# Optimization experiments

Hardware: AMD Instinct MI355X
Metric: run time of the kernel (lower is better)

## Reference

```python
import jax, jax.numpy as jnp
import numpy as np

MARGIN = 0.5
POS_WEIGHT = 0.5
NEG_WEIGHT = 0.5
PUNISHMENT_SCALE = 2.0
POS_THRESHOLD = 0.6
NEG_THRESHOLD = 0.3
BIG = 1e9  # finite sentinel instead of inf (grad-safe under where)


def setup_inputs() -> dict:
    key = jax.random.key(0)
    k1, k2, k3 = jax.random.split(key, 3)
    N, D = 8192, 256
    embeddings = jax.random.normal(k1, (N, D), dtype=jnp.float32)
    labels = jax.random.randint(k2, (N,), 0, 2, dtype=jnp.int32)
    pids = jax.random.randint(k3, (N,), 0, 256, dtype=jnp.int32)
    return {"embeddings": embeddings, "labels": labels, "pids": pids}


def reference(embeddings, labels, pids):
    N = embeddings.shape[0]
    # F.normalize(p=2, dim=1): x / max(||x||, eps)
    norm = jnp.maximum(jnp.linalg.norm(embeddings, axis=1, keepdims=True), 1e-12)
    normed = embeddings / norm
    sim = normed @ normed.T  # (N, N) cosine similarity

    same_pid = pids[:, None] == pids[None, :]            # (N, N)
    genuine_j = (labels == 1)[None, :]                   # (1, N)
    not_self = ~jnp.eye(N, dtype=bool)
    pos_mask = same_pid & genuine_j & not_self           # same pid, genuine, not anchor
    neg_mask = (same_pid & ~genuine_j) | ~same_pid       # same-pid forgeries or cross-pid

    valid = (labels == 1) & pos_mask.any(axis=1) & neg_mask.any(axis=1)

    # hardest positive = min similarity among positives
    hp = jnp.min(jnp.where(pos_mask, sim, BIG), axis=1)  # (N,)

    # semi-hard negatives: hp - margin < sim < hp
    semi = neg_mask & (sim < hp[:, None]) & (sim > (hp - MARGIN)[:, None])
    cand = neg_mask & (sim > hp[:, None])                # harder-than-positive negatives
    hn_semi = jnp.max(jnp.where(semi, sim, -BIG), axis=1)
    hn_cand = jnp.max(jnp.where(cand, sim, -BIG), axis=1)
    hn_all = jnp.max(jnp.where(neg_mask, sim, -BIG), axis=1)
    hn = jnp.where(semi.any(axis=1), hn_semi,
                   jnp.where(cand.any(axis=1), hn_cand, hn_all))

    base = jax.nn.relu(hn - hp + MARGIN)
    weight = jnp.where((hp < POS_THRESHOLD) | (hn > NEG_THRESHOLD),
                       PUNISHMENT_SCALE, 1.0)
    loss = base * weight + POS_WEIGHT * (1.0 - hp) + NEG_WEIGHT * jax.nn.relu(hn + 0.2)

    cnt = jnp.sum(valid)
    total = jnp.sum(jnp.where(valid, loss, 0.0))
    return jnp.where(cnt > 0, total / jnp.maximum(cnt, 1), 0.0)
```

## Files before the change

### kernel.cpp

```cpp
#include <hip/hip_runtime.h>
#include <hip/hip_bf16.h>
#include <stdint.h>

typedef __attribute__((ext_vector_type(8))) short short8;
typedef __attribute__((ext_vector_type(4))) float f32x4;

#define BIGF 1e9f
#define NSLOT 64
#define MAXM 96

__device__ inline float blo(unsigned int u) {
    union { unsigned int i; float f; } v; v.i = u << 16; return v.f;
}
__device__ inline float bhi(unsigned int u) {
    union { unsigned int i; float f; } v; v.i = u & 0xffff0000u; return v.f;
}
__device__ inline unsigned int fkey(float s) {
    unsigned int b = __float_as_uint(s);
    return (b & 0x80000000u) ? ~b : (b | 0x80000000u);
}
__device__ inline float funkey(unsigned int k) {
    unsigned int b = (k & 0x80000000u) ? (k & 0x7fffffffu) : ~k;
    return __uint_as_float(b);
}
__device__ inline void async16(const unsigned short* g, unsigned short* l) {
    __builtin_amdgcn_global_load_lds(
        (const __attribute__((address_space(1))) void*)g,
        (__attribute__((address_space(3))) void*)l, 16, 0, 0);
}
__device__ inline unsigned short f2b(float x) {
    __hip_bfloat16 h = __float2bfloat16(x);
    return *reinterpret_cast<unsigned short*>(&h);
}

__global__ __launch_bounds__(256) void k_normalize(
    const float* __restrict__ emb, const int* __restrict__ labels,
    const int* __restrict__ pids, unsigned short* __restrict__ normed,
    int* __restrict__ gpid, float* __restrict__ hp_init,
    float* __restrict__ gred, int* __restrict__ done)
{
    if (blockIdx.x == 0 && threadIdx.x < 3) {
        if (threadIdx.x < 2) gred[threadIdx.x] = 0.f;
        else *done = 0;
    }
    int w = threadIdx.x >> 6, lane = threadIdx.x & 63;
    int row = blockIdx.x * 4 + w;
    const float4* src = (const float4*)(emb + ((size_t)row << 8));
    float4 x = src[lane];
    float ss = x.x * x.x + x.y * x.y + x.z * x.z + x.w * x.w;
    #pragma unroll
    for (int off = 32; off >= 1; off >>= 1) ss += __shfl_xor(ss, off, 64);
    float inv = 1.0f / fmaxf(sqrtf(ss), 1e-12f);
    ushort4 o;
    o.x = f2b(x.x * inv); o.y = f2b(x.y * inv);
    o.z = f2b(x.z * inv); o.w = f2b(x.w * inv);
    ((ushort4*)(normed + ((size_t)row << 8)))[lane] = o;
    if (lane == 0) {
        gpid[row] = (labels[row] == 1) ? pids[row] : -1;
        hp_init[row] = BIGF;
    }
}

__global__ __launch_bounds__(256) void k_hp_pid(
    const unsigned short* __restrict__ normed, const int* __restrict__ labels,
    const int* __restrict__ pids, float* __restrict__ hp_out, int N, int D)
{
    __shared__ int list[MAXM];
    __shared__ unsigned int hp_loc[MAXM];
    __shared__ unsigned short rows[MAXM * 256];
    __shared__ int cnt;
    int p = blockIdx.x;
    int t = threadIdx.x;
    if (t == 0) cnt = 0;
    __syncthreads();
    for (int j = t; j < N; j += 256)
        if (pids[j] == p && labels[j] == 1) {
            int idx = atomicAdd(&cnt, 1);
            if (idx < MAXM) list[idx] = j;
        }
    __syncthreads();
    int M = min(cnt, MAXM);
    for (int s = t; s < M; s += 256) hp_loc[s] = 0xFFFFFFFFu;
    for (int idx = t; idx < M * 32; idx += 256) {
        int mi = idx >> 5, ch = idx & 31;
        ((uint4*)&rows[mi * 256])[ch] =
            ((const uint4*)(normed + ((size_t)list[mi] << 8)))[ch];
    }
    __syncthreads();
    for (int pr = t; pr < M * M; pr += 256) {
        int i = pr / M, j = pr - i * M;
        if (i == j) continue;
        const uint4* ap = (const uint4*)&rows[i * 256];
        const uint4* bp = (const uint4*)&rows[j * 256];
        float s = 0.f;
        #pragma unroll 4
        for (int k = 0; k < 32; ++k) {
            uint4 a = ap[k], b = bp[k];
            s += blo(a.x) * blo(b.x) + bhi(a.x) * bhi(b.x);
            s += blo(a.y) * blo(b.y) + bhi(a.y) * bhi(b.y);
            s += blo(a.z) * blo(b.z) + bhi(a.z) * bhi(b.z);
            s += blo(a.w) * blo(b.w) + bhi(a.w) * bhi(b.w);
        }
        atomicMin(&hp_loc[i], fkey(s));
    }
    __syncthreads();
    for (int s = t; s < M; s += 256) {
        unsigned int key = hp_loc[s];
        hp_out[list[s]] = (key == 0xFFFFFFFFu) ? BIGF : funkey(key);
    }
}

__global__ __launch_bounds__(256) void k_pass2(
    const unsigned short* __restrict__ normed, const int* __restrict__ pids,
    const int* __restrict__ gpid, const float* __restrict__ hp,
    float* __restrict__ p_hnall, float* __restrict__ p_mbel, int N)
{
    const int b = blockIdx.x;
    int rt = (int)floorf((129.0f - sqrtf(16641.0f - 8.0f * (float)b)) * 0.5f);
    rt = min(rt, 63);
    while (64 * (rt + 1) - ((rt + 1) * rt) / 2 <= b) ++rt;
    while (64 * rt - (rt * (rt - 1)) / 2 > b) --rt;
    const int ct = rt + (b - (64 * rt - (rt * (rt - 1)) / 2));
    const bool diag = (ct == rt);

    __shared__ unsigned short As[2][128 * 32];
    __shared__ unsigned short Bs[2][128 * 32];
    __shared__ float hp_r[128], hp_c[128];
    __shared__ int pid_r[128], gpid_r[128], pid_c[128], gpid_c[128];
    __shared__ unsigned int red1[128], red2[128], red3[128], red4[128];

    const int t = threadIdx.x;
    const int lane = t & 63;
    const int w = t >> 6;
    const int wr = w & 1, wc = w >> 1;
    const int quad = lane >> 4, l16 = lane & 15;
    const int rbase = rt * 128, cbase = ct * 128;

    if (t < 128) {
        hp_r[t] = hp[rbase + t];
        pid_r[t] = pids[rbase + t];
        gpid_r[t] = gpid[rbase + t];
        hp_c[t] = hp[cbase + t];
        pid_c[t] = pids[cbase + t];
        gpid_c[t] = gpid[cbase + t];
        red1[t] = 0u; red2[t] = 0u; red3[t] = 0u; red4[t] = 0u;
    }

    const int r0 = t >> 2, p0 = t & 3;
    const int c0 = p0 ^ ((r0 >> 1) & 3);
    const unsigned short* gA0 = normed + ((size_t)(rbase + r0) << 8) + c0 * 8;
    const unsigned short* gA1 = normed + ((size_t)(rbase + r0 + 64) << 8) + c0 * 8;
    const unsigned short* gB0 = normed + ((size_t)(cbase + r0) << 8) + c0 * 8;
    const unsigned short* gB1 = normed + ((size_t)(cbase + r0 + 64) << 8) + c0 * 8;

    async16(gA0, &As[0][t * 8]);
    async16(gA1, &As[0][2048 + t * 8]);
    if (!diag) {
        async16(gB0, &Bs[0][t * 8]);
        async16(gB1, &Bs[0][2048 + t * 8]);
    }

    f32x4 acc[4][4];
    #pragma unroll
    for (int mt = 0; mt < 4; ++mt)
        #pragma unroll
        for (int nt = 0; nt < 4; ++nt)
            acc[mt][nt] = (f32x4){0.f, 0.f, 0.f, 0.f};

    const int sw = (l16 >> 1) & 3;
    const int aoff = (wr * 64 + l16) * 32 + (quad ^ sw) * 8;
    const int boff = (wc * 64 + l16) * 32 + (quad ^ sw) * 8;

    const unsigned short* Bbase[2] = { diag ? &As[0][0] : &Bs[0][0],
                                       diag ? &As[1][0] : &Bs[1][0] };

    for (int kb = 0; kb < 8; ++kb) {
        __syncthreads();
        int cur = kb & 1;
        if (kb < 7) {
            int nxt = cur ^ 1;
            int ko = (kb + 1) << 5;
            async16(gA0 + ko, &As[nxt][t * 8]);
            async16(gA1 + ko, &As[nxt][2048 + t * 8]);
            if (!diag) {
                async16(gB0 + ko, &Bs[nxt][t * 8]);
                async16(gB1 + ko, &Bs[nxt][2048 + t * 8]);
            }
        }
        short8 af[4], bf[4];
        #pragma unroll
        for (int mt = 0; mt < 4; ++mt)
            af[mt] = *reinterpret_cast<const short8*>(&As[cur][aoff + mt * 512]);
        #pragma unroll
        for (int nt = 0; nt < 4; ++nt)
            bf[nt] = *reinterpret_cast<const short8*>(&Bbase[cur][boff + nt * 512]);
        #pragma unroll
        for (int mt = 0; mt < 4; ++mt)
            #pragma unroll
            for (int nt = 0; nt < 4; ++nt)
                acc[mt][nt] = __builtin_amdgcn_mfma_f32_16x16x32_bf16(
                    af[mt], bf[nt], acc[mt][nt], 0, 0, 0);
    }

    int gp[4];
    #pragma unroll
    for (int nt = 0; nt < 4; ++nt) gp[nt] = gpid_c[wc * 64 + nt * 16 + l16];
    #pragma unroll
    for (int mt = 0; mt < 4; ++mt) {
        #pragma unroll
        for (int r = 0; r < 4; ++r) {
            int rl = wr * 64 + mt * 16 + quad * 4 + r;
            int prow = pid_r[rl];
            float hprow = hp_r[rl];
            float v1 = -BIGF, v2 = -BIGF;
            #pragma unroll
            for (int nt = 0; nt < 4; ++nt) {
                float s = acc[mt][nt][r];
                float tt = (prow != gp[nt]) ? s : -BIGF;
                v1 = fmaxf(v1, tt);
                float t2 = (tt < hprow) ? tt : -BIGF;
                v2 = fmaxf(v2, t2);
            }
            #pragma unroll
            for (int off = 8; off >= 1; off >>= 1) {
                v1 = fmaxf(v1, __shfl_xor(v1, off, 64));
                v2 = fmaxf(v2, __shfl_xor(v2, off, 64));
            }
            if (l16 == 0) {
                atomicMax(&red1[rl], fkey(v1));
                atomicMax(&red2[rl], fkey(v2));
            }
        }
    }

    if (!diag) {
        int4 gr[4];
        #pragma unroll
        for (int mt = 0; mt < 4; ++mt)
            gr[mt] = *(const int4*)&gpid_r[wr * 64 + mt * 16 + quad * 4];
        #pragma unroll
        for (int nt = 0; nt < 4; ++nt) {
            int c = wc * 64 + nt * 16 + l16;
            int pc = pid_c[c];
            float hpc = hp_c[c];
            float v1 = -BIGF, v2 = -BIGF;
            #pragma unroll
            for (int mt = 0; mt < 4; ++mt) {
                const int* g = (const int*)&gr[mt];
                #pragma unroll
                for (int r = 0; r < 4; ++r) {
                    float s = acc[mt][nt][r];
                    float tt = (pc != g[r]) ? s : -BIGF;
                    v1 = fmaxf(v1, tt);
                    float t2 = (tt < hpc) ? tt : -BIGF;
                    v2 = fmaxf(v2, t2);
                }
            }
            v1 = fmaxf(v1, __shfl_xor(v1, 16, 64));
            v1 = fmaxf(v1, __shfl_xor(v1, 32, 64));
            v2 = fmaxf(v2, __shfl_xor(v2, 16, 64));
            v2 = fmaxf(v2, __shfl_xor(v2, 32, 64));
            if (quad == 0) {
                atomicMax(&red3[c], fkey(v1));
                atomicMax(&red4[c], fkey(v2));
            }
        }
    }

    __syncthreads();
    if (t < 128) {
        p_hnall[(size_t)ct * N + rbase + t] = funkey(red1[t]);
        p_mbel[(size_t)ct * N + rbase + t] = funkey(red2[t]);
        if (!diag) {
            p_hnall[(size_t)rt * N + cbase + t] = funkey(red3[t]);
            p_mbel[(size_t)rt * N + cbase + t] = funkey(red4[t]);
        }
    }
}

__global__ __launch_bounds__(256) void k_rowloss(
    const float* __restrict__ hp, const float* __restrict__ p_hnall,
    const float* __restrict__ p_mbel, const int* __restrict__ labels,
    float* __restrict__ gred, int* __restrict__ done,
    float* __restrict__ out, int N)
{
    int i = blockIdx.x * 256 + threadIdx.x;
    float hn_all = -BIGF, mb = -BIGF;
    #pragma unroll 8
    for (int s = 0; s < NSLOT; ++s) {
        hn_all = fmaxf(hn_all, p_hnall[(size_t)s * N + i]);
        mb = fmaxf(mb, p_mbel[(size_t)s * N + i]);
    }
    float hpv = hp[i];
    bool valid = (labels[i] == 1) && (hpv < 1e8f) && (hn_all > -1e8f);
    float hn = (mb > hpv - 0.5f) ? mb : hn_all;
    float base = fmaxf(hn - hpv + 0.5f, 0.f);
    float wgt = (hpv < 0.6f || hn > 0.3f) ? 2.f : 1.f;
    float loss = base * wgt + 0.5f * (1.f - hpv) + 0.5f * fmaxf(hn + 0.2f, 0.f);
    float lsum = valid ? loss : 0.f;
    float lcnt = valid ? 1.f : 0.f;
    #pragma unroll
    for (int off = 32; off >= 1; off >>= 1) {
        lsum += __shfl_xor(lsum, off, 64);
        lcnt += __shfl_xor(lcnt, off, 64);
    }
    __shared__ float rs[4], rc[4];
    int wv = threadIdx.x >> 6, lane = threadIdx.x & 63;
    if (lane == 0) { rs[wv] = lsum; rc[wv] = lcnt; }
    __syncthreads();
    if (threadIdx.x == 0) {
        atomicAdd(&gred[0], rs[0] + rs[1] + rs[2] + rs[3]);
        atomicAdd(&gred[1], rc[0] + rc[1] + rc[2] + rc[3]);
        __threadfence();
        int old = atomicAdd(done, 1);
        if (old == (int)gridDim.x - 1) {
            float S = atomicAdd(&gred[0], 0.f);
            float C = atomicAdd(&gred[1], 0.f);
            out[0] = (C > 0.f) ? S / fmaxf(C, 1.f) : 0.f;
        }
    }
}

extern "C" void kernel_launch(void* const* d_in, const int* in_sizes, int n_in,
                              void* d_out, int out_size, void* d_ws, size_t ws_size,
                              hipStream_t stream)
{
    const float* emb = (const float*)d_in[0];
    const int* labels = (const int*)d_in[1];
    const int* pids = (const int*)d_in[2];
    float* out = (float*)d_out;
    int N = in_sizes[1];
    int D = in_sizes[0] / N;

    char* ws = (char*)d_ws;
    unsigned short* normed = (unsigned short*)ws;  ws += (size_t)N * D * 2;
    int* gpid = (int*)ws;                          ws += (size_t)N * 4;
    float* hp = (float*)ws;                        ws += (size_t)N * 4;
    float* p_hnall = (float*)ws;                   ws += (size_t)N * NSLOT * 4;
    float* p_mbel = (float*)ws;                    ws += (size_t)N * NSLOT * 4;
    float* gred = (float*)ws;                      ws += 2 * 4;
    int* done = (int*)ws;                          ws += 4;

    int M = N / 128;
    int tri = M * (M + 1) / 2;

    k_normalize<<<N / 4, 256, 0, stream>>>(emb, labels, pids, normed, gpid, hp,
                                           gred, done);
    k_hp_pid<<<256, 256, 0, stream>>>(normed, labels, pids, hp, N, D);
    k_pass2<<<tri, 256, 0, stream>>>(normed, pids, gpid, hp,
                                     p_hnall, p_mbel, N);
    k_rowloss<<<N / 256, 256, 0, stream>>>(hp, p_hnall, p_mbel, labels,
                                           gred, done, out, N);
}
```

Measured before the change: 150.0 us.

## Fuse normalize with per-pid hardest-positive and fold row loss into pass2

After: 196.8 us. 1.31x slower.

```diff
diff --git a/kernel.cpp b/kernel.cpp
--- a/kernel.cpp
+++ b/kernel.cpp
@@ -6,7 +6,6 @@
 typedef __attribute__((ext_vector_type(4))) float f32x4;
 
 #define BIGF 1e9f
-#define NSLOT 64
 #define MAXM 96
 
 __device__ inline float blo(unsigned int u) {
@@ -33,44 +32,48 @@
     return *reinterpret_cast<unsigned short*>(&h);
 }
 
-__global__ __launch_bounds__(256) void k_normalize(
+__global__ __launch_bounds__(256) void k_prep(
     const float* __restrict__ emb, const int* __restrict__ labels,
     const int* __restrict__ pids, unsigned short* __restrict__ normed,
-    int* __restrict__ gpid, float* __restrict__ hp_init,
-    float* __restrict__ gred, int* __restrict__ done)
-{
-    if (blockIdx.x == 0 && threadIdx.x < 3) {
-        if (threadIdx.x < 2) gred[threadIdx.x] = 0.f;
-        else *done = 0;
-    }
-    int w = threadIdx.x >> 6, lane = threadIdx.x & 63;
-    int row = blockIdx.x * 4 + w;
-    const float4* src = (const float4*)(emb + ((size_t)row << 8));
-    float4 x = src[lane];
-    float ss = x.x * x.x + x.y * x.y + x.z * x.z + x.w * x.w;
-    #pragma unroll
-    for (int off = 32; off >= 1; off >>= 1) ss += __shfl_xor(ss, off, 64);
-    float inv = 1.0f / fmaxf(sqrtf(ss), 1e-12f);
-    ushort4 o;
-    o.x = f2b(x.x * inv); o.y = f2b(x.y * inv);
-    o.z = f2b(x.z * inv); o.w = f2b(x.w * inv);
-    ((ushort4*)(normed + ((size_t)row << 8)))[lane] = o;
-    if (lane == 0) {
-        gpid[row] = (labels[row] == 1) ? pids[row] : -1;
-        hp_init[row] = BIGF;
-    }
-}
-
-__global__ __launch_bounds__(256) void k_hp_pid(
-    const unsigned short* __restrict__ normed, const int* __restrict__ labels,
-    const int* __restrict__ pids, float* __restrict__ hp_out, int N, int D)
+    int* __restrict__ gpid, float* __restrict__ hp_out,
+    unsigned int* __restrict__ hn_key, unsigned int* __restrict__ mb_key,
+    int* __restrict__ done, int N)
 {
     __shared__ int list[MAXM];
     __shared__ unsigned int hp_loc[MAXM];
     __shared__ unsigned short rows[MAXM * 256];
     __shared__ int cnt;
-    int p = blockIdx.x;
-    int t = threadIdx.x;
+
+    const int b = blockIdx.x;
+    const int t = threadIdx.x;
+    const int nblk = N / 4;
+    const int w = t >> 6, lane = t & 63;
+
+    if (b < nblk) {
+        if (b == 0 && t == 0) *done = 0;
+        if (b < 32) hn_key[b * 256 + t] = 0u;
+        else if (b < 64) mb_key[(b - 32) * 256 + t] = 0u;
+
+        int row = b * 4 + w;
+        const float4* src = (const float4*)(emb + ((size_t)row << 8));
+        float4 x = src[lane];
+        float ss = x.x * x.x + x.y * x.y + x.z * x.z + x.w * x.w;
+        #pragma unroll
+        for (int off = 32; off >= 1; off >>= 1) ss += __shfl_xor(ss, off, 64);
+        float inv = 1.0f / fmaxf(sqrtf(ss), 1e-12f);
+        ushort4 o;
+        o.x = f2b(x.x * inv); o.y = f2b(x.y * inv);
+        o.z = f2b(x.z * inv); o.w = f2b(x.w * inv);
+        ((ushort4*)(normed + ((size_t)row << 8)))[lane] = o;
+        if (lane == 0) {
+            int genuine = (labels[row] == 1);
+            gpid[row] = genuine ? pids[row] : -1;
+            if (!genuine) hp_out[row] = BIGF;
+        }
+        return;
+    }
+
+    int p = b - nblk;
     if (t == 0) cnt = 0;
     __syncthreads();
     for (int j = t; j < N; j += 256)
@@ -81,10 +84,17 @@
     __syncthreads();
     int M = min(cnt, MAXM);
     for (int s = t; s < M; s += 256) hp_loc[s] = 0xFFFFFFFFu;
-    for (int idx = t; idx < M * 32; idx += 256) {
-        int mi = idx >> 5, ch = idx & 31;
-        ((uint4*)&rows[mi * 256])[ch] =
-            ((const uint4*)(normed + ((size_t)list[mi] << 8)))[ch];
+    for (int mi = w; mi < M; mi += 4) {
+        const float4* src = (const float4*)(emb + ((size_t)list[mi] << 8));
+        float4 x = src[lane];
+        float ss = x.x * x.x + x.y * x.y + x.z * x.z + x.w * x.w;
+        #pragma unroll
+        for (int off = 32; off >= 1; off >>= 1) ss += __shfl_xor(ss, off, 64);
+        float inv = 1.0f / fmaxf(sqrtf(ss), 1e-12f);
+        ushort4 o;
+        o.x = f2b(x.x * inv); o.y = f2b(x.y * inv);
+        o.z = f2b(x.z * inv); o.w = f2b(x.w * inv);
+        ((ushort4*)&rows[mi * 256])[lane] = o;
     }
     __syncthreads();
     for (int pr = t; pr < M * M; pr += 256) {
@@ -95,11 +105,11 @@
         float s = 0.f;
         #pragma unroll 4
         for (int k = 0; k < 32; ++k) {
-            uint4 a = ap[k], b = bp[k];
-            s += blo(a.x) * blo(b.x) + bhi(a.x) * bhi(b.x);
-            s += blo(a.y) * blo(b.y) + bhi(a.y) * bhi(b.y);
-            s += blo(a.z) * blo(b.z) + bhi(a.z) * bhi(b.z);
-            s += blo(a.w) * blo(b.w) + bhi(a.w) * bhi(b.w);
+            uint4 a = ap[k], bb = bp[k];
+            s += blo(a.x) * blo(bb.x) + bhi(a.x) * bhi(bb.x);
+            s += blo(a.y) * blo(bb.y) + bhi(a.y) * bhi(bb.y);
+            s += blo(a.z) * blo(bb.z) + bhi(a.z) * bhi(bb.z);
+            s += blo(a.w) * blo(bb.w) + bhi(a.w) * bhi(bb.w);
         }
         atomicMin(&hp_loc[i], fkey(s));
     }
@@ -113,7 +123,9 @@
 __global__ __launch_bounds__(256) void k_pass2(
     const unsigned short* __restrict__ normed, const int* __restrict__ pids,
     const int* __restrict__ gpid, const float* __restrict__ hp,
-    float* __restrict__ p_hnall, float* __restrict__ p_mbel, int N)
+    const int* __restrict__ labels,
+    unsigned int* __restrict__ hn_key, unsigned int* __restrict__ mb_key,
+    int* __restrict__ done, float* __restrict__ out, int N)
 {
     const int b = blockIdx.x;
     int rt = (int)floorf((129.0f - sqrtf(16641.0f - 8.0f * (float)b)) * 0.5f);
@@ -127,7 +139,8 @@
     __shared__ unsigned short Bs[2][128 * 32];
     __shared__ float hp_r[128], hp_c[128];
     __shared__ int pid_r[128], gpid_r[128], pid_c[128], gpid_c[128];
-    __shared__ unsigned int red1[128], red2[128], red3[128], red4[128];
+    __shared__ int amlast;
+    __shared__ float rs[4], rc[4];
 
     const int t = threadIdx.x;
     const int lane = t & 63;
@@ -143,7 +156,6 @@
         hp_c[t] = hp[cbase + t];
         pid_c[t] = pids[cbase + t];
         gpid_c[t] = gpid[cbase + t];
-        red1[t] = 0u; red2[t] = 0u; red3[t] = 0u; red4[t] = 0u;
     }
 
     const int r0 = t >> 2, p0 = t & 3;
@@ -227,8 +239,8 @@
                 v2 = fmaxf(v2, __shfl_xor(v2, off, 64));
             }
             if (l16 == 0) {
-                atomicMax(&red1[rl], fkey(v1));
-                atomicMax(&red2[rl], fkey(v2));
+                atomicMax(&hn_key[rbase + rl], fkey(v1));
+                atomicMax(&mb_key[rbase + rl], fkey(v2));
             }
         }
     }
@@ -261,63 +273,42 @@
             v2 = fmaxf(v2, __shfl_xor(v2, 16, 64));
             v2 = fmaxf(v2, __shfl_xor(v2, 32, 64));
             if (quad == 0) {
-                atomicMax(&red3[c], fkey(v1));
-                atomicMax(&red4[c], fkey(v2));
-            }
-        }
-    }
-
-    __syncthreads();
-    if (t < 128) {
-        p_hnall[(size_t)ct * N + rbase + t] = funkey(red1[t]);
-        p_mbel[(size_t)ct * N + rbase + t] = funkey(red2[t]);
-        if (!diag) {
-            p_hnall[(size_t)rt * N + cbase + t] = funkey(red3[t]);
-            p_mbel[(size_t)rt * N + cbase + t] = funkey(red4[t]);
-        }
-    }
-}
-
-__global__ __launch_bounds__(256) void k_rowloss(
-    const float* __restrict__ hp, const float* __restrict__ p_hnall,
-    const float* __restrict__ p_mbel, const int* __restrict__ labels,
-    float* __restrict__ gred, int* __restrict__ done,
-    float* __restrict__ out, int N)
-{
-    int i = blockIdx.x * 256 + threadIdx.x;
-    float hn_all = -BIGF, mb = -BIGF;
-    #pragma unroll 8
-    for (int s = 0; s < NSLOT; ++s) {
-        hn_all = fmaxf(hn_all, p_hnall[(size_t)s * N + i]);
-        mb = fmaxf(mb, p_mbel[(size_t)s * N + i]);
-    }
-    float hpv = hp[i];
-    bool valid = (labels[i] == 1) && (hpv < 1e8f) && (hn_all > -1e8f);
-    float hn = (mb > hpv - 0.5f) ? mb : hn_all;
-    float base = fmaxf(hn - hpv + 0.5f, 0.f);
-    float wgt = (hpv < 0.6f || hn > 0.3f) ? 2.f : 1.f;
-    float loss = base * wgt + 0.5f * (1.f - hpv) + 0.5f * fmaxf(hn + 0.2f, 0.f);
-    float lsum = valid ? loss : 0.f;
-    float lcnt = valid ? 1.f : 0.f;
+                atomicMax(&hn_key[cbase + c], fkey(v1));
+                atomicMax(&mb_key[cbase + c], fkey(v2));
+            }
+        }
+    }
+
+    if (t == 0) {
+        __threadfence();
+        amlast = (atomicAdd(done, 1) == (int)gridDim.x - 1);
+    }
+    __syncthreads();
+    if (!amlast) return;
+
+    float lsum = 0.f, lcnt = 0.f;
+    for (int i = t; i < N; i += 256) {
+        float hn_all = funkey(atomicMax(&hn_key[i], 0u));
+        float mb = funkey(atomicMax(&mb_key[i], 0u));
+        float hpv = hp[i];
+        bool valid = (labels[i] == 1) && (hpv < 1e8f) && (hn_all > -1e8f);
+        float hn = (mb > hpv - 0.5f) ? mb : hn_all;
+        float base = fmaxf(hn - hpv + 0.5f, 0.f);
+        float wgt = (hpv < 0.6f || hn > 0.3f) ? 2.f : 1.f;
+        float loss = base * wgt + 0.5f * (1.f - hpv) + 0.5f * fmaxf(hn + 0.2f, 0.f);
+        if (valid) { lsum += loss; lcnt += 1.f; }
+    }
     #pragma unroll
     for (int off = 32; off >= 1; off >>= 1) {
         lsum += __shfl_xor(lsum, off, 64);
         lcnt += __shfl_xor(lcnt, off, 64);
     }
-    __shared__ float rs[4], rc[4];
-    int wv = threadIdx.x >> 6, lane = threadIdx.x & 63;
-    if (lane == 0) { rs[wv] = lsum; rc[wv] = lcnt; }
-    __syncthreads();
-    if (threadIdx.x == 0) {
-        atomicAdd(&gred[0], rs[0] + rs[1] + rs[2] + rs[3]);
-        atomicAdd(&gred[1], rc[0] + rc[1] + rc[2] + rc[3]);
-        __threadfence();
-        int old = atomicAdd(done, 1);
-        if (old == (int)gridDim.x - 1) {
-            float S = atomicAdd(&gred[0], 0.f);
-            float C = atomicAdd(&gred[1], 0.f);
-            out[0] = (C > 0.f) ? S / fmaxf(C, 1.f) : 0.f;
-        }
+    if (lane == 0) { rs[w] = lsum; rc[w] = lcnt; }
+    __syncthreads();
+    if (t == 0) {
+        float S = rs[0] + rs[1] + rs[2] + rs[3];
+        float C = rc[0] + rc[1] + rc[2] + rc[3];
+        out[0] = (C > 0.f) ? S / fmaxf(C, 1.f) : 0.f;
     }
 }
 
@@ -330,25 +321,20 @@
     const int* pids = (const int*)d_in[2];
     float* out = (float*)d_out;
     int N = in_sizes[1];
-    int D = in_sizes[0] / N;
 
     char* ws = (char*)d_ws;
-    unsigned short* normed = (unsigned short*)ws;  ws += (size_t)N * D * 2;
+    unsigned short* normed = (unsigned short*)ws;  ws += (size_t)N * 256 * 2;
     int* gpid = (int*)ws;                          ws += (size_t)N * 4;
     float* hp = (float*)ws;                        ws += (size_t)N * 4;
-    float* p_hnall = (float*)ws;                   ws += (size_t)N * NSLOT * 4;
-    float* p_mbel = (float*)ws;                    ws += (size_t)N * NSLOT * 4;
-    float* gred = (float*)ws;                      ws += 2 * 4;
+    unsigned int* hn_key = (unsigned int*)ws;      ws += (size_t)N * 4;
+    unsigned int* mb_key = (unsigned int*)ws;      ws += (size_t)N * 4;
     int* done = (int*)ws;                          ws += 4;
 
     int M = N / 128;
     int tri = M * (M + 1) / 2;
 
-    k_normalize<<<N / 4, 256, 0, stream>>>(emb, labels, pids, normed, gpid, hp,
-                                           gred, done);
-    k_hp_pid<<<256, 256, 0, stream>>>(normed, labels, pids, hp, N, D);
-    k_pass2<<<tri, 256, 0, stream>>>(normed, pids, gpid, hp,
-                                     p_hnall, p_mbel, N);
-    k_rowloss<<<N / 256, 256, 0, stream>>>(hp, p_hnall, p_mbel, labels,
-                                           gred, done, out, N);
-}
+    k_prep<<<N / 4 + 256, 256, 0, stream>>>(emb, labels, pids, normed, gpid,
+                                            hp, hn_key, mb_key, done, N);
+    k_pass2<<<tri, 256, 0, stream>>>(normed, pids, gpid, hp, labels,
+                                     hn_key, mb_key, done, out, N);
+}
```
